# Optimization experiments

Measured on AMD Instinct MI355X. Metric: run time of the kernel, lower is better.

## Reference

```python
import math
import jax, jax.numpy as jnp
import numpy as np

B, LQ, LK, D, DV = 16, 2048, 2048, 256, 256


def setup_inputs() -> dict:
    key = jax.random.key(0)
    k1, k2, k3, k4 = jax.random.split(key, 4)
    query = jax.random.normal(k1, (B, LQ, D), dtype=jnp.float32)
    kmat = jax.random.normal(k2, (B, LK, D), dtype=jnp.float32)
    value = jax.random.normal(k3, (B, LK, DV), dtype=jnp.float32)
    # per-batch valid lengths in [1, LK] (avoid 0 => all -inf row)
    valid_len = jax.random.randint(k4, (B,), 1, LK + 1, dtype=jnp.int64)
    return {"query": query, "key": kmat, "value": value, "valid_len": valid_len}


def reference(query, key, value, valid_len):
    d = query.shape[-1]
    # [B, Lq, Lk] scaled dot-product scores
    scores = jnp.einsum("bqd,bkd->bqk", query, key) / math.sqrt(d)
    # mask positions k >= valid_len[b] (same mask broadcast over all queries,
    # matching the repeat(1, Lq).view(shape) in the original masked_softmax)
    mask = jnp.arange(key.shape[1])[None, None, :] < valid_len[:, None, None]
    scores = jnp.where(mask, scores, -jnp.inf)
    attn = jax.nn.softmax(scores, axis=-1)  # dropout rate is 0.0 => identity
    return jnp.einsum("bqk,bkv->bqv", attn, value)
```

## Files before the change

kernel.cpp:

```cpp
#include <hip/hip_runtime.h>
#include <hip/hip_bf16.h>

#define B_   16
#define LQ_  2048
#define LK_  2048
#define D_   256
#define DV_  256
#define QB   64
#define NW   4

typedef __bf16 bf16x8_t __attribute__((ext_vector_type(8)));
typedef short  s16x8    __attribute__((ext_vector_type(8)));
typedef short  s16x4    __attribute__((ext_vector_type(4)));
typedef float  f32x4    __attribute__((ext_vector_type(4)));

__device__ __forceinline__ unsigned short f2bf(float f) {
  unsigned int u = __builtin_bit_cast(unsigned int, f);
  u += 0x7fffu + ((u >> 16) & 1u);
  return (unsigned short)(u >> 16);
}

__device__ __forceinline__ s16x8 pack8(float4 a, float4 b) {
  s16x8 r;
  r[0] = (short)f2bf(a.x); r[1] = (short)f2bf(a.y);
  r[2] = (short)f2bf(a.z); r[3] = (short)f2bf(a.w);
  r[4] = (short)f2bf(b.x); r[5] = (short)f2bf(b.y);
  r[6] = (short)f2bf(b.z); r[7] = (short)f2bf(b.w);
  return r;
}

__device__ __forceinline__ void glds16(const unsigned short* g, unsigned short* l) {
  __builtin_amdgcn_global_load_lds(
      (const __attribute__((address_space(1))) unsigned int*)g,
      (__attribute__((address_space(3))) unsigned int*)l, 16, 0, 0);
}

__global__ __launch_bounds__(256) void prep_k(const float* __restrict__ K,
                                              unsigned short* __restrict__ wsK) {
  int gid = blockIdx.x * 256 + threadIdx.x;
  int gr = gid >> 5;
  int c  = gid & 31;
  const float* src = K + ((size_t)gr << 8) + c * 8;
  float4 a = *(const float4*)(src);
  float4 b = *(const float4*)(src + 4);
  *(s16x8*)(wsK + ((size_t)gr << 8) + ((c ^ (gr & 7)) << 3)) = pack8(a, b);
}

__global__ __launch_bounds__(256) void prep_v(const float* __restrict__ V,
                                              unsigned short* __restrict__ wsV) {
  __shared__ unsigned short t[256 * 40];
  const int tid = threadIdx.x;
  const float* src = V + (size_t)blockIdx.x * 32 * 256;
  #pragma unroll
  for (int i = 0; i < 8; ++i) {
    int idx = i * 256 + tid;
    int k   = idx >> 6;
    int dv0 = (idx & 63) * 4;
    float4 x = *(const float4*)(src + k * 256 + dv0);
    t[(dv0 + 0) * 40 + k] = f2bf(x.x);
    t[(dv0 + 1) * 40 + k] = f2bf(x.y);
    t[(dv0 + 2) * 40 + k] = f2bf(x.z);
    t[(dv0 + 3) * 40 + k] = f2bf(x.w);
  }
  __syncthreads();
  unsigned short* dst = wsV + (size_t)blockIdx.x * 8192;
  #pragma unroll
  for (int i = 0; i < 4; ++i) {
    int idx = i * 256 + tid;
    int dv = idx >> 2;
    int cs = idx & 3;
    int c2 = cs ^ ((dv >> 1) & 3);
    s16x8 v = *(const s16x8*)(&t[dv * 40 + cs * 8]);
    *(s16x8*)(dst + dv * 32 + c2 * 8) = v;
  }
}

__global__ __launch_bounds__(256) void attn_fwd2(
    const float* __restrict__ Q, const unsigned short* __restrict__ wsK,
    const unsigned short* __restrict__ wsV, const int* __restrict__ VL,
    float* __restrict__ O) {
  __shared__ __align__(16) unsigned short lds_k[2][32 * 256];
  __shared__ __align__(16) unsigned short lds_v[2][256 * 32];
  __shared__ __align__(16) unsigned short lds_p[NW][16 * 32];

  const int tid  = threadIdx.x;
  const int wid  = tid >> 6;
  const int lane = tid & 63;
  const int l15  = lane & 15;
  const int lg   = lane >> 4;

  const int bid = blockIdx.x;
  const int b   = bid >> 5;
  const int qt  = bid & 31;

  int n_k = (VL[1] == 0) ? VL[2 * b] : VL[b];
  if (n_k < 1) n_k = 1;
  if (n_k > LK_) n_k = LK_;
  const int nt = (n_k + 31) >> 5;

  const int qbase = qt * QB + wid * 16;

  s16x8 qf[8];
  {
    const float* qp = Q + ((size_t)b * LQ_ + qbase + l15) * D_ + lg * 8;
    #pragma unroll
    for (int dk = 0; dk < 8; ++dk) {
      float4 a = *(const float4*)(qp + dk * 32);
      float4 c = *(const float4*)(qp + dk * 32 + 4);
      qf[dk] = pack8(a, c);
    }
  }

  f32x4 o[16];
  #pragma unroll
  for (int c = 0; c < 16; ++c) o[c] = (f32x4){0.f, 0.f, 0.f, 0.f};
  float m[4]    = {-INFINITY, -INFINITY, -INFINITY, -INFINITY};
  float lsum[4] = {0.f, 0.f, 0.f, 0.f};

  const unsigned short* kb  = wsK + (size_t)b * LK_ * D_;
  const unsigned short* vbw = wsV + (size_t)b * 64 * 8192;

  {
    const unsigned short* ks = kb;
    const unsigned short* vs = vbw;
    #pragma unroll
    for (int p = 0; p < 4; ++p) {
      int it = p * 256 + wid * 64;
      glds16(ks + (size_t)(it + lane) * 8, &lds_k[0][it * 8]);
      glds16(vs + (size_t)(it + lane) * 8, &lds_v[0][it * 8]);
    }
  }
  __syncthreads();

  for (int t = 0; t < nt; ++t) {
    const int cur = t & 1;
    if (t + 1 < nt) {
      const unsigned short* ks = kb  + (size_t)(t + 1) * 8192;
      const unsigned short* vs = vbw + (size_t)(t + 1) * 8192;
      #pragma unroll
      for (int p = 0; p < 4; ++p) {
        int it = p * 256 + wid * 64;
        glds16(ks + (size_t)(it + lane) * 8, &lds_k[cur ^ 1][it * 8]);
        glds16(vs + (size_t)(it + lane) * 8, &lds_v[cur ^ 1][it * 8]);
      }
    }

    f32x4 s[2];
    #pragma unroll
    for (int kc = 0; kc < 2; ++kc) {
      f32x4 acc = (f32x4){0.f, 0.f, 0.f, 0.f};
      int krow = kc * 16 + l15;
      int sw = (krow & 7) << 3;
      #pragma unroll
      for (int dk = 0; dk < 8; ++dk) {
        int off = krow * 256 + ((dk * 32 + lg * 8) ^ sw);
        s16x8 kf = *(const s16x8*)(&lds_k[cur][off]);
        acc = __builtin_amdgcn_mfma_f32_16x16x32_bf16(
            __builtin_bit_cast(bf16x8_t, qf[dk]),
            __builtin_bit_cast(bf16x8_t, kf), acc, 0, 0, 0);
      }
      s[kc] = acc;
    }

    #pragma unroll
    for (int kc = 0; kc < 2; ++kc) {
      int gk = t * 32 + kc * 16 + l15;
      #pragma unroll
      for (int j = 0; j < 4; ++j) {
        float v = s[kc][j] * 0.0625f;
        s[kc][j] = (gk < n_k) ? v : -INFINITY;
      }
    }

    float pm[4];
    #pragma unroll
    for (int j = 0; j < 4; ++j) pm[j] = fmaxf(s[0][j], s[1][j]);
    #pragma unroll
    for (int off = 1; off < 16; off <<= 1) {
      #pragma unroll
      for (int j = 0; j < 4; ++j)
        pm[j] = fmaxf(pm[j], __shfl_xor(pm[j], off, 64));
    }
    int need = 0;
    #pragma unroll
    for (int j = 0; j < 4; ++j) need |= (pm[j] > m[j] + 8.0f) ? 1 : 0;
    if (__any(need)) {
      #pragma unroll
      for (int j = 0; j < 4; ++j) {
        float mn = fmaxf(m[j], pm[j]);
        float sc = __expf(m[j] - mn);
        m[j] = mn;
        lsum[j] *= sc;
        #pragma unroll
        for (int c = 0; c < 16; ++c) o[c][j] *= sc;
      }
    }

    float psum[4] = {0.f, 0.f, 0.f, 0.f};
    #pragma unroll
    for (int kc = 0; kc < 2; ++kc) {
      #pragma unroll
      for (int j = 0; j < 4; ++j) {
        float p = __expf(s[kc][j] - m[j]);
        psum[j] += p;
        int r = lg * 4 + j;
        int col = kc * 16 + l15;
        int ke = col ^ (((r >> 1) & 3) << 3);
        lds_p[wid][r * 32 + ke] = f2bf(p);
      }
    }
    #pragma unroll
    for (int off = 1; off < 16; off <<= 1) {
      #pragma unroll
      for (int j = 0; j < 4; ++j)
        psum[j] += __shfl_xor(psum[j], off, 64);
    }
    #pragma unroll
    for (int j = 0; j < 4; ++j) lsum[j] += psum[j];

    s16x8 pa = *(const s16x8*)(&lds_p[wid][l15 * 32 + ((lg ^ ((l15 >> 1) & 3)) << 3)]);

    #pragma unroll
    for (int c = 0; c < 16; ++c) {
      int dv = c * 16 + l15;
      int off = dv * 32 + ((lg ^ ((dv >> 1) & 3)) << 3);
      s16x8 vf = *(const s16x8*)(&lds_v[cur][off]);
      o[c] = __builtin_amdgcn_mfma_f32_16x16x32_bf16(
          __builtin_bit_cast(bf16x8_t, pa),
          __builtin_bit_cast(bf16x8_t, vf), o[c], 0, 0, 0);
    }

    __syncthreads();
  }

  float inv[4];
  #pragma unroll
  for (int j = 0; j < 4; ++j) inv[j] = 1.0f / lsum[j];
  float* ob = O + ((size_t)b * LQ_ + qbase) * DV_;
  #pragma unroll
  for (int c = 0; c < 16; ++c) {
    #pragma unroll
    for (int j = 0; j < 4; ++j) {
      int r = lg * 4 + j;
      ob[(size_t)r * DV_ + c * 16 + l15] = o[c][j] * inv[j];
    }
  }
}

__global__ __launch_bounds__(256) void attn_fwd(
    const float* __restrict__ Q, const float* __restrict__ K,
    const float* __restrict__ V, const int* __restrict__ VL,
    float* __restrict__ O) {
  __shared__ __align__(16) unsigned short lds_k[64 * D_];
  __shared__ __align__(16) unsigned short lds_v[DV_ * 64];
  __shared__ __align__(16) unsigned short lds_p[NW][16 * 64];

  const int tid  = threadIdx.x;
  const int wid  = tid >> 6;
  const int lane = tid & 63;
  const int l15  = lane & 15;
  const int lg   = lane >> 4;
  const int bid = blockIdx.x;
  const int b   = bid >> 5;
  const int qt  = bid & 31;

  int n_k = (VL[1] == 0) ? VL[2 * b] : VL[b];
  if (n_k < 1) n_k = 1;
  if (n_k > LK_) n_k = LK_;

  const int qbase = qt * QB + wid * 16;
  s16x8 qf[8];
  {
    const float* qp = Q + ((size_t)b * LQ_ + qbase + l15) * D_ + lg * 8;
    #pragma unroll
    for (int dk = 0; dk < 8; ++dk) {
      float4 a = *(const float4*)(qp + dk * 32);
      float4 c = *(const float4*)(qp + dk * 32 + 4);
      qf[dk] = pack8(a, c);
    }
  }
  f32x4 o[16];
  #pragma unroll
  for (int c = 0; c < 16; ++c) o[c] = (f32x4){0.f, 0.f, 0.f, 0.f};
  float m[4]    = {-INFINITY, -INFINITY, -INFINITY, -INFINITY};
  float lsum[4] = {0.f, 0.f, 0.f, 0.f};
  const float* kb = K + (size_t)b * LK_ * D_;
  const float* vb = V + (size_t)b * LK_ * DV_;
  const int nt = (n_k + 63) / 64;

  for (int kt = 0; kt < nt; ++kt) {
    __syncthreads();
    {
      const float* src = kb + (size_t)kt * 64 * D_;
      #pragma unroll
      for (int p = 0; p < 8; ++p) {
        int e = (p * 256 + tid) * 8;
        int r = e >> 8;
        int d = e & 255;
        float4 a = *(const float4*)(src + e);
        float4 c = *(const float4*)(src + e + 4);
        int off = r * 256 + (d ^ ((r & 7) << 3));
        *(s16x8*)(&lds_k[off]) = pack8(a, c);
      }
    }
    {
      const float* src = vb + (size_t)kt * 64 * DV_;
      #pragma unroll
      for (int p = 0; p < 2; ++p) {
        int item = p * 256 + tid;
        int k0  = (item >> 5) * 4;
        int dv0 = (item & 31) * 8;
        float va[4][8];
        #pragma unroll
        for (int r = 0; r < 4; ++r) {
          float4 x = *(const float4*)(src + (k0 + r) * DV_ + dv0);
          float4 y = *(const float4*)(src + (k0 + r) * DV_ + dv0 + 4);
          va[r][0]=x.x; va[r][1]=x.y; va[r][2]=x.z; va[r][3]=x.w;
          va[r][4]=y.x; va[r][5]=y.y; va[r][6]=y.z; va[r][7]=y.w;
        }
        #pragma unroll
        for (int i = 0; i < 8; ++i) {
          int dv = dv0 + i;
          s16x4 w;
          w[0]=(short)f2bf(va[0][i]); w[1]=(short)f2bf(va[1][i]);
          w[2]=(short)f2bf(va[2][i]); w[3]=(short)f2bf(va[3][i]);
          int off = dv * 64 + (k0 ^ ((dv & 7) << 3));
          *(s16x4*)(&lds_v[off]) = w;
        }
      }
    }
    __syncthreads();

    f32x4 s[4];
    #pragma unroll
    for (int kc = 0; kc < 4; ++kc) {
      f32x4 acc = (f32x4){0.f, 0.f, 0.f, 0.f};
      int krow = kc * 16 + l15;
      int sw = (krow & 7) << 3;
      #pragma unroll
      for (int dk = 0; dk < 8; ++dk) {
        int off = krow * 256 + ((dk * 32 + lg * 8) ^ sw);
        s16x8 kf = *(const s16x8*)(&lds_k[off]);
        acc = __builtin_amdgcn_mfma_f32_16x16x32_bf16(
            __builtin_bit_cast(bf16x8_t, qf[dk]),
            __builtin_bit_cast(bf16x8_t, kf), acc, 0, 0, 0);
      }
      s[kc] = acc;
    }
    #pragma unroll
    for (int kc = 0; kc < 4; ++kc) {
      int gk = kt * 64 + kc * 16 + l15;
      #pragma unroll
      for (int j = 0; j < 4; ++j) {
        float v = s[kc][j] * 0.0625f;
        s[kc][j] = (gk < n_k) ? v : -INFINITY;
      }
    }
    float pm[4];
    #pragma unroll
    for (int j = 0; j < 4; ++j)
      pm[j] = fmaxf(fmaxf(s[0][j], s[1][j]), fmaxf(s[2][j], s[3][j]));
    #pragma unroll
    for (int off = 1; off < 16; off <<= 1) {
      #pragma unroll
      for (int j = 0; j < 4; ++j)
        pm[j] = fmaxf(pm[j], __shfl_xor(pm[j], off, 64));
    }
    float sc[4];
    #pragma unroll
    for (int j = 0; j < 4; ++j) {
      float mn = fmaxf(m[j], pm[j]);
      sc[j] = __expf(m[j] - mn);
      m[j] = mn;
    }
    float psum[4] = {0.f, 0.f, 0.f, 0.f};
    #pragma unroll
    for (int kc = 0; kc < 4; ++kc) {
      #pragma unroll
      for (int j = 0; j < 4; ++j) {
        float p = __expf(s[kc][j] - m[j]);
        psum[j] += p;
        int r = lg * 4 + j;
        int col = kc * 16 + l15;
        lds_p[wid][r * 64 + (col ^ ((r & 7) << 3))] = f2bf(p);
      }
    }
    #pragma unroll
    for (int off = 1; off < 16; off <<= 1) {
      #pragma unroll
      for (int j = 0; j < 4; ++j)
        psum[j] += __shfl_xor(psum[j], off, 64);
    }
    #pragma unroll
    for (int j = 0; j < 4; ++j) lsum[j] = lsum[j] * sc[j] + psum[j];
    #pragma unroll
    for (int c = 0; c < 16; ++c) {
      #pragma unroll
      for (int j = 0; j < 4; ++j) o[c][j] *= sc[j];
    }
    s16x8 pa[2];
    #pragma unroll
    for (int kk = 0; kk < 2; ++kk) {
      int r = l15;
      int k = kk * 32 + lg * 8;
      pa[kk] = *(const s16x8*)(&lds_p[wid][r * 64 + (k ^ ((r & 7) << 3))]);
    }
    #pragma unroll
    for (int c = 0; c < 16; ++c) {
      #pragma unroll
      for (int kk = 0; kk < 2; ++kk) {
        int dv = c * 16 + l15;
        int k = kk * 32 + lg * 8;
        s16x8 vf = *(const s16x8*)(&lds_v[dv * 64 + (k ^ ((dv & 7) << 3))]);
        o[c] = __builtin_amdgcn_mfma_f32_16x16x32_bf16(
            __builtin_bit_cast(bf16x8_t, pa[kk]),
            __builtin_bit_cast(bf16x8_t, vf), o[c], 0, 0, 0);
      }
    }
  }
  float inv[4];
  #pragma unroll
  for (int j = 0; j < 4; ++j) inv[j] = 1.0f / lsum[j];
  float* ob = O + ((size_t)b * LQ_ + qbase) * DV_;
  #pragma unroll
  for (int c = 0; c < 16; ++c) {
    #pragma unroll
    for (int j = 0; j < 4; ++j) {
      int r = lg * 4 + j;
      ob[(size_t)r * DV_ + c * 16 + l15] = o[c][j] * inv[j];
    }
  }
}

extern "C" void kernel_launch(void* const* d_in, const int* in_sizes, int n_in,
                              void* d_out, int out_size, void* d_ws, size_t ws_size,
                              hipStream_t stream) {
  const float* Q  = (const float*)d_in[0];
  const float* K  = (const float*)d_in[1];
  const float* V  = (const float*)d_in[2];
  const int*   VL = (const int*)d_in[3];
  float* O = (float*)d_out;

  const size_t kv_elems = (size_t)B_ * LK_ * D_;
  const size_t need = kv_elems * 2 * sizeof(unsigned short);
  if (ws_size >= need) {
    unsigned short* wsK = (unsigned short*)d_ws;
    unsigned short* wsV = wsK + kv_elems;
    prep_k<<<dim3(4096), dim3(256), 0, stream>>>(K, wsK);
    prep_v<<<dim3(1024), dim3(256), 0, stream>>>(V, wsV);
    attn_fwd2<<<dim3(512), dim3(256), 0, stream>>>(Q, wsK, wsV, VL, O);
  } else {
    attn_fwd<<<dim3(512), dim3(256), 0, stream>>>(Q, K, V, VL, O);
  }
}
```

Measured before the change: 168.0 us.

## Split key tiles across two wave groups with 512-thread blocks and merge softmax states

The main kernel now runs 8 waves per block. Two groups of four waves each take half of a 64-key tile, with per-row softmax state and a final cross-group merge of max, sum and output through LDS. QK^T is computed with the operands swapped so each lane holds a single row max and sum. P is passed to the PV matmul through lane shuffles instead of an LDS round trip. It also adds s_setprio around the MFMA blocks and widens the V prep layout to 64-key tiles. The aim is more waves in flight and fewer LDS and sync costs per key. The cost is a larger LDS footprint (128KB), which limits occupancy, plus an epilogue merge.

```diff
diff --git a/kernel.cpp b/kernel.cpp
--- a/kernel.cpp
+++ b/kernel.cpp
@@ -6,8 +6,7 @@
 #define LK_  2048
 #define D_   256
 #define DV_  256
-#define QB   64
-#define NW   4
+#define MINF -1.0e30f
 
 typedef __bf16 bf16x8_t __attribute__((ext_vector_type(8)));
 typedef short  s16x8    __attribute__((ext_vector_type(8)));
@@ -48,46 +47,45 @@
 
 __global__ __launch_bounds__(256) void prep_v(const float* __restrict__ V,
                                               unsigned short* __restrict__ wsV) {
-  __shared__ unsigned short t[256 * 40];
+  __shared__ unsigned short t[256 * 72];
   const int tid = threadIdx.x;
-  const float* src = V + (size_t)blockIdx.x * 32 * 256;
-  #pragma unroll
-  for (int i = 0; i < 8; ++i) {
+  const float* src = V + (size_t)blockIdx.x * 64 * 256;
+  #pragma unroll
+  for (int i = 0; i < 16; ++i) {
     int idx = i * 256 + tid;
     int k   = idx >> 6;
     int dv0 = (idx & 63) * 4;
     float4 x = *(const float4*)(src + k * 256 + dv0);
-    t[(dv0 + 0) * 40 + k] = f2bf(x.x);
-    t[(dv0 + 1) * 40 + k] = f2bf(x.y);
-    t[(dv0 + 2) * 40 + k] = f2bf(x.z);
-    t[(dv0 + 3) * 40 + k] = f2bf(x.w);
+    t[(dv0 + 0) * 72 + k] = f2bf(x.x);
+    t[(dv0 + 1) * 72 + k] = f2bf(x.y);
+    t[(dv0 + 2) * 72 + k] = f2bf(x.z);
+    t[(dv0 + 3) * 72 + k] = f2bf(x.w);
   }
   __syncthreads();
-  unsigned short* dst = wsV + (size_t)blockIdx.x * 8192;
-  #pragma unroll
-  for (int i = 0; i < 4; ++i) {
+  unsigned short* dst = wsV + (size_t)blockIdx.x * 16384;
+  #pragma unroll
+  for (int i = 0; i < 8; ++i) {
     int idx = i * 256 + tid;
-    int dv = idx >> 2;
-    int cs = idx & 3;
-    int c2 = cs ^ ((dv >> 1) & 3);
-    s16x8 v = *(const s16x8*)(&t[dv * 40 + cs * 8]);
-    *(s16x8*)(dst + dv * 32 + c2 * 8) = v;
-  }
-}
-
-__global__ __launch_bounds__(256) void attn_fwd2(
+    int dv = idx >> 3;
+    int ch = idx & 7;
+    s16x8 v = *(const s16x8*)(&t[dv * 72 + ch * 8]);
+    *(s16x8*)(dst + dv * 64 + ((ch ^ (dv & 7)) << 3)) = v;
+  }
+}
+
+__global__ __launch_bounds__(512) void attn_fwd3(
     const float* __restrict__ Q, const unsigned short* __restrict__ wsK,
     const unsigned short* __restrict__ wsV, const int* __restrict__ VL,
     float* __restrict__ O) {
-  __shared__ __align__(16) unsigned short lds_k[2][32 * 256];
-  __shared__ __align__(16) unsigned short lds_v[2][256 * 32];
-  __shared__ __align__(16) unsigned short lds_p[NW][16 * 32];
+  __shared__ __align__(16) unsigned short lds_s[4][16384];
 
   const int tid  = threadIdx.x;
   const int wid  = tid >> 6;
   const int lane = tid & 63;
   const int l15  = lane & 15;
   const int lg   = lane >> 4;
+  const int rg   = wid & 3;
+  const int kh   = wid >> 2;
 
   const int bid = blockIdx.x;
   const int b   = bid >> 5;
@@ -96,9 +94,9 @@
   int n_k = (VL[1] == 0) ? VL[2 * b] : VL[b];
   if (n_k < 1) n_k = 1;
   if (n_k > LK_) n_k = LK_;
-  const int nt = (n_k + 31) >> 5;
-
-  const int qbase = qt * QB + wid * 16;
+  const int nt = (n_k + 63) >> 6;
+
+  const int qbase = qt * 64 + rg * 16;
 
   s16x8 qf[8];
   {
@@ -114,137 +112,151 @@
   f32x4 o[16];
   #pragma unroll
   for (int c = 0; c < 16; ++c) o[c] = (f32x4){0.f, 0.f, 0.f, 0.f};
-  float m[4]    = {-INFINITY, -INFINITY, -INFINITY, -INFINITY};
-  float lsum[4] = {0.f, 0.f, 0.f, 0.f};
-
-  const unsigned short* kb  = wsK + (size_t)b * LK_ * D_;
-  const unsigned short* vbw = wsV + (size_t)b * 64 * 8192;
-
-  {
-    const unsigned short* ks = kb;
-    const unsigned short* vs = vbw;
-    #pragma unroll
-    for (int p = 0; p < 4; ++p) {
-      int it = p * 256 + wid * 64;
-      glds16(ks + (size_t)(it + lane) * 8, &lds_k[0][it * 8]);
-      glds16(vs + (size_t)(it + lane) * 8, &lds_v[0][it * 8]);
-    }
-  }
+  float m = MINF, l = 0.f;
+
+  const unsigned short* kbw = wsK + (size_t)b * LK_ * D_;
+  const unsigned short* vbw = wsV + (size_t)b * LK_ * DV_;
+
+#define STAGE(buf, t) do {                                                   \
+    const unsigned short* ks_ = kbw + (size_t)(t) * 16384;                   \
+    const unsigned short* vs_ = vbw + (size_t)(t) * 16384;                   \
+    _Pragma("unroll")                                                        \
+    for (int p = 0; p < 4; ++p) {                                            \
+      int cu = p * 512 + wid * 64;                                           \
+      glds16(ks_ + (size_t)(cu + lane) * 8, &lds_s[(buf)][cu * 8]);          \
+      glds16(vs_ + (size_t)(cu + lane) * 8, &lds_s[2 + (buf)][cu * 8]);      \
+    }                                                                        \
+  } while (0)
+
+  STAGE(0, 0);
   __syncthreads();
 
   for (int t = 0; t < nt; ++t) {
     const int cur = t & 1;
-    if (t + 1 < nt) {
-      const unsigned short* ks = kb  + (size_t)(t + 1) * 8192;
-      const unsigned short* vs = vbw + (size_t)(t + 1) * 8192;
-      #pragma unroll
-      for (int p = 0; p < 4; ++p) {
-        int it = p * 256 + wid * 64;
-        glds16(ks + (size_t)(it + lane) * 8, &lds_k[cur ^ 1][it * 8]);
-        glds16(vs + (size_t)(it + lane) * 8, &lds_v[cur ^ 1][it * 8]);
-      }
-    }
-
+    if (t + 1 < nt) STAGE(cur ^ 1, t + 1);
+
+    const unsigned short* kl = &lds_s[cur][0];
     f32x4 s[2];
+    __builtin_amdgcn_s_setprio(1);
     #pragma unroll
     for (int kc = 0; kc < 2; ++kc) {
-      f32x4 acc = (f32x4){0.f, 0.f, 0.f, 0.f};
-      int krow = kc * 16 + l15;
+      int krow = kh * 32 + kc * 16 + l15;
       int sw = (krow & 7) << 3;
-      #pragma unroll
-      for (int dk = 0; dk < 8; ++dk) {
-        int off = krow * 256 + ((dk * 32 + lg * 8) ^ sw);
-        s16x8 kf = *(const s16x8*)(&lds_k[cur][off]);
-        acc = __builtin_amdgcn_mfma_f32_16x16x32_bf16(
-            __builtin_bit_cast(bf16x8_t, qf[dk]),
-            __builtin_bit_cast(bf16x8_t, kf), acc, 0, 0, 0);
-      }
-      s[kc] = acc;
-    }
+      const unsigned short* base = kl + krow * 256;
+      f32x4 a0 = (f32x4){0.f, 0.f, 0.f, 0.f};
+      f32x4 a1 = (f32x4){0.f, 0.f, 0.f, 0.f};
+      #pragma unroll
+      for (int dk = 0; dk < 4; ++dk) {
+        s16x8 k0 = *(const s16x8*)(base + ((dk * 64 + lg * 8) ^ sw));
+        s16x8 k1 = *(const s16x8*)(base + ((dk * 64 + 32 + lg * 8) ^ sw));
+        a0 = __builtin_amdgcn_mfma_f32_16x16x32_bf16(
+            __builtin_bit_cast(bf16x8_t, k0),
+            __builtin_bit_cast(bf16x8_t, qf[2 * dk]), a0, 0, 0, 0);
+        a1 = __builtin_amdgcn_mfma_f32_16x16x32_bf16(
+            __builtin_bit_cast(bf16x8_t, k1),
+            __builtin_bit_cast(bf16x8_t, qf[2 * dk + 1]), a1, 0, 0, 0);
+      }
+      s[kc] = a0 + a1;
+    }
+    __builtin_amdgcn_s_setprio(0);
 
     #pragma unroll
     for (int kc = 0; kc < 2; ++kc) {
-      int gk = t * 32 + kc * 16 + l15;
+      int gk = t * 64 + kh * 32 + kc * 16 + lg * 4;
+      #pragma unroll
+      for (int j = 0; j < 4; ++j)
+        s[kc][j] = (gk + j < n_k) ? s[kc][j] * 0.0625f : MINF;
+    }
+
+    float pm = s[0][0];
+    pm = fmaxf(pm, s[0][1]); pm = fmaxf(pm, s[0][2]); pm = fmaxf(pm, s[0][3]);
+    pm = fmaxf(pm, s[1][0]); pm = fmaxf(pm, s[1][1]);
+    pm = fmaxf(pm, s[1][2]); pm = fmaxf(pm, s[1][3]);
+    pm = fmaxf(pm, __shfl_xor(pm, 16, 64));
+    pm = fmaxf(pm, __shfl_xor(pm, 32, 64));
+    if (__any(pm > m + 8.0f)) {
+      float mn = fmaxf(m, pm);
+      float sc = __expf(m - mn);
+      m = mn; l *= sc;
+      #pragma unroll
+      for (int c = 0; c < 16; ++c) o[c] = o[c] * sc;
+    }
+    float p0[4], p1[4];
+    #pragma unroll
+    for (int j = 0; j < 4; ++j) {
+      p0[j] = __expf(s[0][j] - m);
+      p1[j] = __expf(s[1][j] - m);
+    }
+    float ps = ((p0[0] + p0[1]) + (p0[2] + p0[3]))
+             + ((p1[0] + p1[1]) + (p1[2] + p1[3]));
+    ps += __shfl_xor(ps, 16, 64);
+    ps += __shfl_xor(ps, 32, 64);
+    l += ps;
+
+    float pv8[8];
+    int sl0 = l15 + ((lg & 1) ? 32 : 0);
+    #pragma unroll
+    for (int h = 0; h < 2; ++h) {
+      int sl = sl0 + h * 16;
       #pragma unroll
       for (int j = 0; j < 4; ++j) {
-        float v = s[kc][j] * 0.0625f;
-        s[kc][j] = (gk < n_k) ? v : -INFINITY;
-      }
-    }
-
-    float pm[4];
-    #pragma unroll
-    for (int j = 0; j < 4; ++j) pm[j] = fmaxf(s[0][j], s[1][j]);
-    #pragma unroll
-    for (int off = 1; off < 16; off <<= 1) {
-      #pragma unroll
-      for (int j = 0; j < 4; ++j)
-        pm[j] = fmaxf(pm[j], __shfl_xor(pm[j], off, 64));
-    }
-    int need = 0;
-    #pragma unroll
-    for (int j = 0; j < 4; ++j) need |= (pm[j] > m[j] + 8.0f) ? 1 : 0;
-    if (__any(need)) {
-      #pragma unroll
-      for (int j = 0; j < 4; ++j) {
-        float mn = fmaxf(m[j], pm[j]);
-        float sc = __expf(m[j] - mn);
-        m[j] = mn;
-        lsum[j] *= sc;
-        #pragma unroll
-        for (int c = 0; c < 16; ++c) o[c][j] *= sc;
-      }
-    }
-
-    float psum[4] = {0.f, 0.f, 0.f, 0.f};
-    #pragma unroll
-    for (int kc = 0; kc < 2; ++kc) {
-      #pragma unroll
-      for (int j = 0; j < 4; ++j) {
-        float p = __expf(s[kc][j] - m[j]);
-        psum[j] += p;
-        int r = lg * 4 + j;
-        int col = kc * 16 + l15;
-        int ke = col ^ (((r >> 1) & 3) << 3);
-        lds_p[wid][r * 32 + ke] = f2bf(p);
-      }
-    }
-    #pragma unroll
-    for (int off = 1; off < 16; off <<= 1) {
-      #pragma unroll
-      for (int j = 0; j < 4; ++j)
-        psum[j] += __shfl_xor(psum[j], off, 64);
-    }
-    #pragma unroll
-    for (int j = 0; j < 4; ++j) lsum[j] += psum[j];
-
-    s16x8 pa = *(const s16x8*)(&lds_p[wid][l15 * 32 + ((lg ^ ((l15 >> 1) & 3)) << 3)]);
-
+        float a  = __shfl(p0[j], sl, 64);
+        float bb = __shfl(p1[j], sl, 64);
+        pv8[h * 4 + j] = (lg >= 2) ? bb : a;
+      }
+    }
+    s16x8 pb;
+    #pragma unroll
+    for (int e = 0; e < 8; ++e) pb[e] = (short)f2bf(pv8[e]);
+
+    const unsigned short* vl_ = &lds_s[2 + cur][0];
+    __builtin_amdgcn_s_setprio(1);
     #pragma unroll
     for (int c = 0; c < 16; ++c) {
       int dv = c * 16 + l15;
-      int off = dv * 32 + ((lg ^ ((dv >> 1) & 3)) << 3);
-      s16x8 vf = *(const s16x8*)(&lds_v[cur][off]);
+      int off = dv * 64 + (((kh * 4 + lg) ^ (dv & 7)) << 3);
+      s16x8 vf = *(const s16x8*)(vl_ + off);
       o[c] = __builtin_amdgcn_mfma_f32_16x16x32_bf16(
-          __builtin_bit_cast(bf16x8_t, pa),
-          __builtin_bit_cast(bf16x8_t, vf), o[c], 0, 0, 0);
-    }
+          __builtin_bit_cast(bf16x8_t, vf),
+          __builtin_bit_cast(bf16x8_t, pb), o[c], 0, 0, 0);
+    }
+    __builtin_amdgcn_s_setprio(0);
 
     __syncthreads();
   }
 
-  float inv[4];
-  #pragma unroll
-  for (int j = 0; j < 4; ++j) inv[j] = 1.0f / lsum[j];
-  float* ob = O + ((size_t)b * LQ_ + qbase) * DV_;
-  #pragma unroll
-  for (int c = 0; c < 16; ++c) {
-    #pragma unroll
-    for (int j = 0; j < 4; ++j) {
-      int r = lg * 4 + j;
-      ob[(size_t)r * DV_ + c * 16 + l15] = o[c][j] * inv[j];
-    }
-  }
+  float* mrg = (float*)&lds_s[0][0];
+  float* mo  = mrg + (wid & 3) * 4160;
+  if (wid >= 4) {
+    #pragma unroll
+    for (int c = 0; c < 16; ++c)
+      #pragma unroll
+      for (int j = 0; j < 4; ++j)
+        mo[l15 * 257 + c * 16 + lg * 4 + j] = o[c][j];
+    mo[4112 + l15] = m;
+    mo[4128 + l15] = l;
+  }
+  __syncthreads();
+  if (wid < 4) {
+    float mb = mo[4112 + l15];
+    float lb = mo[4128 + l15];
+    float M  = fmaxf(m, mb);
+    float sa = __expf(m - M), sb = __expf(mb - M);
+    float invL = 1.0f / (sa * l + sb * lb);
+    float* ob = O + ((size_t)b * LQ_ + qbase + l15) * DV_;
+    #pragma unroll
+    for (int c = 0; c < 16; ++c) {
+      int dvb = c * 16 + lg * 4;
+      const float* mr = mo + l15 * 257 + dvb;
+      float4 r;
+      r.x = (sa * o[c][0] + sb * mr[0]) * invL;
+      r.y = (sa * o[c][1] + sb * mr[1]) * invL;
+      r.z = (sa * o[c][2] + sb * mr[2]) * invL;
+      r.w = (sa * o[c][3] + sb * mr[3]) * invL;
+      *(float4*)(ob + dvb) = r;
+    }
+  }
+#undef STAGE
 }
 
 __global__ __launch_bounds__(256) void attn_fwd(
@@ -253,7 +265,7 @@
     float* __restrict__ O) {
   __shared__ __align__(16) unsigned short lds_k[64 * D_];
   __shared__ __align__(16) unsigned short lds_v[DV_ * 64];
-  __shared__ __align__(16) unsigned short lds_p[NW][16 * 64];
+  __shared__ __align__(16) unsigned short lds_p[4][16 * 64];
 
   const int tid  = threadIdx.x;
   const int wid  = tid >> 6;
@@ -268,7 +280,7 @@
   if (n_k < 1) n_k = 1;
   if (n_k > LK_) n_k = LK_;
 
-  const int qbase = qt * QB + wid * 16;
+  const int qbase = qt * 64 + wid * 16;
   s16x8 qf[8];
   {
     const float* qp = Q + ((size_t)b * LQ_ + qbase + l15) * D_ + lg * 8;
@@ -299,8 +311,7 @@
         int d = e & 255;
         float4 a = *(const float4*)(src + e);
         float4 c = *(const float4*)(src + e + 4);
-        int off = r * 256 + (d ^ ((r & 7) << 3));
-        *(s16x8*)(&lds_k[off]) = pack8(a, c);
+        *(s16x8*)(&lds_k[r * 256 + (d ^ ((r & 7) << 3))]) = pack8(a, c);
       }
     }
     {
@@ -324,8 +335,7 @@
           s16x4 w;
           w[0]=(short)f2bf(va[0][i]); w[1]=(short)f2bf(va[1][i]);
           w[2]=(short)f2bf(va[2][i]); w[3]=(short)f2bf(va[3][i]);
-          int off = dv * 64 + (k0 ^ ((dv & 7) << 3));
-          *(s16x4*)(&lds_v[off]) = w;
+          *(s16x4*)(&lds_v[dv * 64 + (k0 ^ ((dv & 7) << 3))]) = w;
         }
       }
     }
@@ -339,8 +349,7 @@
       int sw = (krow & 7) << 3;
       #pragma unroll
       for (int dk = 0; dk < 8; ++dk) {
-        int off = krow * 256 + ((dk * 32 + lg * 8) ^ sw);
-        s16x8 kf = *(const s16x8*)(&lds_k[off]);
+        s16x8 kf = *(const s16x8*)(&lds_k[krow * 256 + ((dk * 32 + lg * 8) ^ sw)]);
         acc = __builtin_amdgcn_mfma_f32_16x16x32_bf16(
             __builtin_bit_cast(bf16x8_t, qf[dk]),
             __builtin_bit_cast(bf16x8_t, kf), acc, 0, 0, 0);
@@ -381,8 +390,7 @@
         float p = __expf(s[kc][j] - m[j]);
         psum[j] += p;
         int r = lg * 4 + j;
-        int col = kc * 16 + l15;
-        lds_p[wid][r * 64 + (col ^ ((r & 7) << 3))] = f2bf(p);
+        lds_p[wid][r * 64 + ((kc * 16 + l15) ^ ((r & 7) << 3))] = f2bf(p);
       }
     }
     #pragma unroll
@@ -400,18 +408,14 @@
     }
     s16x8 pa[2];
     #pragma unroll
-    for (int kk = 0; kk < 2; ++kk) {
-      int r = l15;
-      int k = kk * 32 + lg * 8;
-      pa[kk] = *(const s16x8*)(&lds_p[wid][r * 64 + (k ^ ((r & 7) << 3))]);
-    }
+    for (int kk = 0; kk < 2; ++kk)
+      pa[kk] = *(const s16x8*)(&lds_p[wid][l15 * 64 + ((kk * 32 + lg * 8) ^ ((l15 & 7) << 3))]);
     #pragma unroll
     for (int c = 0; c < 16; ++c) {
       #pragma unroll
       for (int kk = 0; kk < 2; ++kk) {
         int dv = c * 16 + l15;
-        int k = kk * 32 + lg * 8;
-        s16x8 vf = *(const s16x8*)(&lds_v[dv * 64 + (k ^ ((dv & 7) << 3))]);
+        s16x8 vf = *(const s16x8*)(&lds_v[dv * 64 + ((kk * 32 + lg * 8) ^ ((dv & 7) << 3))]);
         o[c] = __builtin_amdgcn_mfma_f32_16x16x32_bf16(
             __builtin_bit_cast(bf16x8_t, pa[kk]),
             __builtin_bit_cast(bf16x8_t, vf), o[c], 0, 0, 0);
@@ -447,8 +451,8 @@
     unsigned short* wsK = (unsigned short*)d_ws;
     unsigned short* wsV = wsK + kv_elems;
     prep_k<<<dim3(4096), dim3(256), 0, stream>>>(K, wsK);
-    prep_v<<<dim3(1024), dim3(256), 0, stream>>>(V, wsV);
-    attn_fwd2<<<dim3(512), dim3(256), 0, stream>>>(Q, wsK, wsV, VL, O);
+    prep_v<<<dim3(512), dim3(256), 0, stream>>>(V, wsV);
+    attn_fwd3<<<dim3(512), dim3(512), 0, stream>>>(Q, wsK, wsV, VL, O);
   } else {
     attn_fwd<<<dim3(512), dim3(256), 0, stream>>>(Q, K, V, VL, O);
   }
```

After: 135.7 us. 19.3% less time.
